# Optimization experiments

Measured on AMD Instinct MI355X. Metric: run time of the kernel, lower is better.

Reference implementation:

```python
import jax, jax.numpy as jnp
import numpy as np

D = 256      # linear_dim
H = 8        # heads
B, S = 4, 2048


def setup_inputs() -> dict:
    key = jax.random.key(0)
    ks = jax.random.split(key, 9)
    scale = 1.0 / np.sqrt(D)
    x = jax.random.normal(ks[0], (B, S, D), dtype=jnp.float32)
    # per-head Linear weights stacked: [H, out, in] (torch Linear layout)
    Wq = jax.random.normal(ks[1], (H, D, D), dtype=jnp.float32) * scale
    bq = jax.random.normal(ks[2], (H, D), dtype=jnp.float32) * scale
    Wk = jax.random.normal(ks[3], (H, D, D), dtype=jnp.float32) * scale
    bk = jax.random.normal(ks[4], (H, D), dtype=jnp.float32) * scale
    Wv = jax.random.normal(ks[5], (H, D, D), dtype=jnp.float32) * scale
    bv = jax.random.normal(ks[6], (H, D), dtype=jnp.float32) * scale
    Wo = jax.random.normal(ks[7], (D, H * D), dtype=jnp.float32) * (1.0 / np.sqrt(H * D))
    bo = jax.random.normal(ks[8], (D,), dtype=jnp.float32) * scale
    return {"x": x, "Wq": Wq, "bq": bq, "Wk": Wk, "bk": bk,
            "Wv": Wv, "bv": bv, "Wo": Wo, "bo": bo}


def reference(x, Wq, bq, Wk, bk, Wv, bv, Wo, bo):
    # Batched per-head projections (torch Linear: y = x @ W.T + b)
    Q = jnp.einsum('bsd,hed->bhse', x, Wq) + bq[None, :, None, :]  # [B,H,S,D]
    K = jnp.einsum('bsd,hed->bhse', x, Wk) + bk[None, :, None, :]
    V = jnp.einsum('bsd,hed->bhse', x, Wv) + bv[None, :, None, :]
    scores = jnp.einsum('bhse,bhte->bhst', Q, K) / jnp.sqrt(jnp.float32(D))  # [B,H,Sq,Sk]
    # FAITHFUL quirk: original softmaxes over dim=1 of [B,S,S] -> the QUERY axis.
    attn = jax.nn.softmax(scores, axis=2)
    Z = jnp.einsum('bhst,bhte->bhse', attn, V)       # [B,H,S,D]
    Z = jnp.transpose(Z, (0, 2, 1, 3)).reshape(B, S, H * D)  # concat heads (head-major order matches torch.cat)
    return jnp.einsum('bsf,of->bso', Z, Wo) + bo
```

## Files before the change

kernel.cpp:

```cpp
#include <hip/hip_runtime.h>
#include <hip/hip_bf16.h>

#define DEV __device__ __forceinline__

typedef __bf16 bf16x8 __attribute__((ext_vector_type(8)));
typedef float f32x4 __attribute__((ext_vector_type(4)));

DEV f32x4 mfma16(bf16x8 a, bf16x8 b, f32x4 c) {
  return __builtin_amdgcn_mfma_f32_16x16x32_bf16(a, b, c, 0, 0, 0);
}

DEV ushort f2bf(float f) {
  union { __hip_bfloat16 h; ushort u; } cv;
  cv.h = __float2bfloat16(f);
  return cv.u;
}
DEV float bf2f(ushort u) {
  union { float f; unsigned v; } cv; cv.v = ((unsigned)u) << 16; return cv.f;
}

DEV float fexp2(float x) { return __builtin_amdgcn_exp2f(x); }

#define GLD16(gp, lp)                                                              \
  __builtin_amdgcn_global_load_lds(                                                \
      (const __attribute__((address_space(1))) unsigned int*)(gp),                 \
      (__attribute__((address_space(3))) unsigned int*)(lp), 16, 0, 0)


__global__ __launch_bounds__(256) void convert_all(
    const float* __restrict__ x, const float* __restrict__ wq,
    const float* __restrict__ wk, const float* __restrict__ wv,
    const float* __restrict__ wo, ushort* __restrict__ dst)
{
  size_t i = ((size_t)blockIdx.x * 256 + threadIdx.x) * 4;
  const float* src; size_t off;
  if (i < (size_t)2097152) { src = x; off = i; }
  else {
    size_t j = i - 2097152;
    unsigned wsel = (unsigned)(j >> 19);
    off = j & 524287;
    src = wsel == 0 ? wq : wsel == 1 ? wk : wsel == 2 ? wv : wo;
  }
  float4 v = *(const float4*)(src + off);
  ushort4 o;
  o.x = f2bf(v.x); o.y = f2bf(v.y); o.z = f2bf(v.z); o.w = f2bf(v.w);
  *(ushort4*)(dst + i) = o;
}

template<int BM, int BN>
__global__ __launch_bounds__(256, 2) void gemm_qkv(
    const ushort* __restrict__ A,
    const ushort* __restrict__ W0, const ushort* __restrict__ W1, const ushort* __restrict__ W2,
    int K,
    const float* __restrict__ b0, const float* __restrict__ b1, const float* __restrict__ b2,
    ushort* __restrict__ Qo, ushort* __restrict__ Ko, ushort* __restrict__ Vo)
{
  constexpr int WM = BM / 2, WN = BN / 2, MF = WM / 16, NF = WN / 16;
  const int n0 = blockIdx.x * BN, m0 = blockIdx.y * BM;
  const int tid = threadIdx.x, lane = tid & 63;
  const int wm = (tid >> 7) & 1, wn = (tid >> 6) & 1;
  const int g = lane >> 4, r15 = lane & 15;

  __shared__ ushort As[BM * 72];
  __shared__ ushort Bs[BN * 72];

  const int p = n0 >> 11;
  const ushort* Bt = (p == 0 ? W0 : p == 1 ? W1 : W2) + (size_t)(n0 & 2047) * K;

  f32x4 acc[MF][NF];
#pragma unroll
  for (int m = 0; m < MF; m++)
#pragma unroll
    for (int n = 0; n < NF; n++) acc[m][n] = (f32x4){0.f, 0.f, 0.f, 0.f};

  for (int k0 = 0; k0 < K; k0 += 64) {
#pragma unroll
    for (int i = 0; i < 4; i++) {
      int ci = tid * 4 + i; int r = ci >> 3, c = ci & 7;
      *(uint4*)&As[r * 72 + c * 8] = *(const uint4*)&A[(size_t)(m0 + r) * K + k0 + c * 8];
      *(uint4*)&Bs[r * 72 + c * 8] = *(const uint4*)&Bt[(size_t)r * K + k0 + c * 8];
    }
    __syncthreads();
    bf16x8 af[MF][2], bfr[NF][2];
#pragma unroll
    for (int m = 0; m < MF; m++)
#pragma unroll
      for (int k2 = 0; k2 < 2; ++k2)
        af[m][k2] = *(const bf16x8*)&As[(wm * WM + m * 16 + r15) * 72 + k2 * 32 + g * 8];
#pragma unroll
    for (int n = 0; n < NF; n++)
#pragma unroll
      for (int k2 = 0; k2 < 2; ++k2)
        bfr[n][k2] = *(const bf16x8*)&Bs[(wn * WN + n * 16 + r15) * 72 + k2 * 32 + g * 8];
#pragma unroll
    for (int k2 = 0; k2 < 2; ++k2)
#pragma unroll
      for (int m = 0; m < MF; m++)
#pragma unroll
        for (int n = 0; n < NF; n++) acc[m][n] = mfma16(af[m][k2], bfr[n][k2], acc[m][n]);
    __syncthreads();
  }

  const float* bias = (p == 0 ? b0 : p == 1 ? b1 : b2);
  const float scl = (p == 0 ? 0.0625f * 1.44269504088896f : 1.0f);
#pragma unroll
  for (int m = 0; m < MF; m++)
#pragma unroll
    for (int n = 0; n < NF; n++)
#pragma unroll
      for (int r = 0; r < 4; r++) {
        int row = m0 + wm * WM + m * 16 + g * 4 + r;
        int col = n0 + wn * WN + n * 16 + r15;
        int ce = col & 2047;
        float v = (acc[m][n][r] + bias[ce]) * scl;
        int b = row >> 11, s = row & 2047, h = ce >> 8, e = ce & 255;
        int bh = b * 8 + h;
        if (p == 0) {
          Qo[((size_t)(bh * 2048 + s) << 8) + e] = f2bf(v);
        } else if (p == 1) {
          int ee = ((((e >> 3) ^ (s & 7)) & 31) << 3) | (e & 7);
          Ko[((size_t)(bh * 2048 + s) << 8) + ee] = f2bf(v);
        } else {
          Vo[(((size_t)bh * 64 + (s >> 5)) << 13) + e * 32 + (s & 31)] = f2bf(v);
        }
      }
}

__global__ __launch_bounds__(256, 2) void gemm_out(
    const ushort* __restrict__ A, const ushort* __restrict__ Bw,
    const float* __restrict__ bias, float* __restrict__ out)
{
  const int n0 = blockIdx.x * 64, m0 = blockIdx.y * 64;
  const int tid = threadIdx.x, lane = tid & 63;
  const int wm = (tid >> 7) & 1, wn = (tid >> 6) & 1;
  const int g = lane >> 4, r15 = lane & 15;

  __shared__ ushort As[64 * 72];
  __shared__ ushort Bs[64 * 72];

  f32x4 acc[2][2];
#pragma unroll
  for (int m = 0; m < 2; m++)
#pragma unroll
    for (int n = 0; n < 2; n++) acc[m][n] = (f32x4){0.f, 0.f, 0.f, 0.f};

  for (int k0 = 0; k0 < 2048; k0 += 64) {
#pragma unroll
    for (int i = 0; i < 2; ++i) {
      int ci = tid * 2 + i, r = ci >> 3, c = ci & 7;
      *(uint4*)&As[r * 72 + c * 8] = *(const uint4*)&A[(size_t)(m0 + r) * 2048 + k0 + c * 8];
      *(uint4*)&Bs[r * 72 + c * 8] = *(const uint4*)&Bw[(size_t)(n0 + r) * 2048 + k0 + c * 8];
    }
    __syncthreads();
    bf16x8 af[2][2], bfr[2][2];
#pragma unroll
    for (int m = 0; m < 2; ++m)
#pragma unroll
      for (int k2 = 0; k2 < 2; ++k2)
        af[m][k2] = *(const bf16x8*)&As[(wm * 32 + m * 16 + r15) * 72 + k2 * 32 + g * 8];
#pragma unroll
    for (int n = 0; n < 2; ++n)
#pragma unroll
      for (int k2 = 0; k2 < 2; ++k2)
        bfr[n][k2] = *(const bf16x8*)&Bs[(wn * 32 + n * 16 + r15) * 72 + k2 * 32 + g * 8];
#pragma unroll
    for (int k2 = 0; k2 < 2; ++k2)
#pragma unroll
      for (int m = 0; m < 2; ++m)
#pragma unroll
        for (int n = 0; n < 2; ++n)
          acc[m][n] = mfma16(af[m][k2], bfr[n][k2], acc[m][n]);
    __syncthreads();
  }

#pragma unroll
  for (int m = 0; m < 2; m++)
#pragma unroll
    for (int n = 0; n < 2; n++)
#pragma unroll
      for (int r = 0; r < 4; r++) {
        int row = m0 + wm * 32 + m * 16 + g * 4 + r;
        int col = n0 + wn * 32 + n * 16 + r15;
        out[(size_t)row * 256 + col] = acc[m][n][r] + bias[col];
      }
}

__global__ __launch_bounds__(256, 2) void attn_p0(
    const ushort* __restrict__ Qb, const ushort* __restrict__ Kb,
    float* __restrict__ lpart)
{
  const int bid = blockIdx.x;
  const int swz = (bid & 7) * 64 + (bid >> 3);
  const int bh = swz >> 4, stile = (swz >> 1) & 7, half = swz & 1;
  const int s0 = stile * 256;
  const int tid = threadIdx.x, lane = tid & 63, w = tid >> 6;
  const int g = lane >> 4, r15 = lane & 15;

  __shared__ __align__(16) ushort Ks[2][8192];

  uint4 qr[4][8];
#pragma unroll
  for (int h = 0; h < 4; ++h) {
    const ushort* qrow = &Qb[((size_t)bh * 2048 + s0 + w * 64 + h * 16 + r15) * 256 + g * 8];
#pragma unroll
    for (int kk = 0; kk < 8; kk++) qr[h][kk] = *(const uint4*)&qrow[kk * 32];
  }
#pragma unroll
  for (int h = 0; h < 4; ++h)
#pragma unroll
    for (int kk = 0; kk < 8; kk++)
      asm volatile("" : "+v"(qr[h][kk].x), "+v"(qr[h][kk].y),
                        "+v"(qr[h][kk].z), "+v"(qr[h][kk].w));

  const ushort* Ktile = Kb + ((size_t)bh << 19);
  const int it0 = half * 32, it1 = it0 + 32;

#pragma unroll
  for (int i = 0; i < 4; ++i)
    GLD16(&Ktile[(size_t)it0 * 8192 + (i * 256 + tid) * 8], &Ks[0][(i * 256 + tid) * 8]);
  asm volatile("s_waitcnt vmcnt(0)" ::: "memory");
  __syncthreads();

  for (int it = it0; it < it1; ++it) {
    const int cur = it & 1;
    if (it < it1 - 1) {
#pragma unroll
      for (int i = 0; i < 4; ++i)
        GLD16(&Ktile[(size_t)(it + 1) * 8192 + (i * 256 + tid) * 8],
              &Ks[cur ^ 1][(i * 256 + tid) * 8]);
    }

#pragma unroll
    for (int n = 0; n < 2; ++n) {
      f32x4 gh[4];
#pragma unroll
      for (int h = 0; h < 4; ++h) gh[h] = (f32x4){0.f, 0.f, 0.f, 0.f};
#pragma unroll
      for (int kk = 0; kk < 8; ++kk) {
        bf16x8 kb = *(const bf16x8*)&Ks[cur][(n * 16 + r15) * 256 + (((kk * 4 + g) ^ (r15 & 7)) << 3)];
        gh[0] = mfma16(*(const bf16x8*)&qr[0][kk], kb, gh[0]);
        gh[1] = mfma16(*(const bf16x8*)&qr[1][kk], kb, gh[1]);
        gh[2] = mfma16(*(const bf16x8*)&qr[2][kk], kb, gh[2]);
        gh[3] = mfma16(*(const bf16x8*)&qr[3][kk], kb, gh[3]);
      }
      float sn = 0.f;
#pragma unroll
      for (int h = 0; h < 4; ++h)
        sn += fexp2(gh[h][0]) + fexp2(gh[h][1]) + fexp2(gh[h][2]) + fexp2(gh[h][3]);
      sn += __shfl_xor(sn, 16);
      sn += __shfl_xor(sn, 32);
      if (g == 0)
        lpart[((size_t)((stile * 4 + w) * 32 + bh) << 11) + it * 32 + n * 16 + r15] = sn;
    }

    asm volatile("s_waitcnt vmcnt(0)" ::: "memory");
    __syncthreads();
  }
}

__global__ __launch_bounds__(256, 2) void attn_p1(
    const ushort* __restrict__ Qb, const ushort* __restrict__ Kb,
    const ushort* __restrict__ Vt, ushort* __restrict__ Zb)
{
  const int bid = blockIdx.x;
  const int swz = (bid & 7) * 64 + (bid >> 3);
  const int bh = swz >> 4, stile = swz & 15;
  const int s0 = stile * 128;
  const int tid = threadIdx.x, lane = tid & 63, w = tid >> 6;
  const int g = lane >> 4, r15 = lane & 15;

  __shared__ __align__(16) ushort Ks[2][8192];
  __shared__ __align__(16) ushort Ps[2][5120];

  bf16x8 q[2][8];
#pragma unroll
  for (int h = 0; h < 2; ++h) {
    const ushort* qrow = &Qb[((size_t)bh * 2048 + s0 + w * 32 + h * 16 + r15) * 256 + g * 8];
#pragma unroll
    for (int kk = 0; kk < 8; kk++) q[h][kk] = *(const bf16x8*)&qrow[kk * 32];
  }

  const ushort* Ktile = Kb + ((size_t)bh << 19);
  const ushort* Vtile = Vt + ((size_t)bh << 19);

  f32x4 acc[8][4];
#pragma unroll
  for (int m = 0; m < 8; m++)
#pragma unroll
    for (int n = 0; n < 4; n++) acc[m][n] = (f32x4){0.f, 0.f, 0.f, 0.f};

#pragma unroll
  for (int i = 0; i < 4; ++i)
    GLD16(&Ktile[(size_t)(i * 256 + tid) * 8], &Ks[0][(i * 256 + tid) * 8]);
  asm volatile("s_waitcnt vmcnt(0)" ::: "memory");
  __syncthreads();

  for (int it = 0; it < 64; ++it) {
    const int cur = it & 1;
    bf16x8 vb[4];
#pragma unroll
    for (int n = 0; n < 4; ++n)
      vb[n] = *(const bf16x8*)&Vtile[(size_t)it * 8192 + (w * 64 + n * 16 + r15) * 32 + g * 8];
    if (it < 63) {
#pragma unroll
      for (int i = 0; i < 4; ++i)
        GLD16(&Ktile[(size_t)(it + 1) * 8192 + (i * 256 + tid) * 8],
              &Ks[cur ^ 1][(i * 256 + tid) * 8]);
    }

#pragma unroll
    for (int h = 0; h < 2; ++h) {
      f32x4 gg[2];
      gg[0] = (f32x4){0.f, 0.f, 0.f, 0.f};
      gg[1] = (f32x4){0.f, 0.f, 0.f, 0.f};
#pragma unroll
      for (int n = 0; n < 2; ++n)
#pragma unroll
        for (int kk = 0; kk < 8; ++kk) {
          bf16x8 kb = *(const bf16x8*)&Ks[cur][(n * 16 + r15) * 256 + (((kk * 4 + g) ^ (r15 & 7)) << 3)];
          gg[n] = mfma16(q[h][kk], kb, gg[n]);
        }
#pragma unroll
      for (int n = 0; n < 2; ++n)
#pragma unroll
        for (int rr = 0; rr < 4; ++rr)
          Ps[cur][(w * 32 + h * 16 + g * 4 + rr) * 40 + n * 16 + r15] = f2bf(fexp2(gg[n][rr]));
    }

    asm volatile("s_waitcnt vmcnt(0)" ::: "memory");
    __syncthreads();

#pragma unroll
    for (int mh = 0; mh < 2; ++mh) {
      bf16x8 pa[4];
#pragma unroll
      for (int m = 0; m < 4; ++m)
        pa[m] = *(const bf16x8*)&Ps[cur][((mh * 4 + m) * 16 + r15) * 40 + g * 8];
#pragma unroll
      for (int n = 0; n < 4; ++n)
#pragma unroll
        for (int m = 0; m < 4; ++m)
          acc[mh * 4 + m][n] = mfma16(pa[m], vb[n], acc[mh * 4 + m][n]);
    }
  }

  const int b = bh >> 3, h = bh & 7;
#pragma unroll
  for (int m = 0; m < 8; m++)
#pragma unroll
    for (int n = 0; n < 4; n++)
#pragma unroll
      for (int rr = 0; rr < 4; rr++) {
        int sl = m * 16 + g * 4 + rr;
        int el = w * 64 + n * 16 + r15;
        Zb[((size_t)(b * 2048 + s0 + sl)) * 2048 + h * 256 + el] = f2bf(acc[m][n][rr]);
      }
}

__global__ __launch_bounds__(256) void vscale(
    ushort* __restrict__ Vt, const float* __restrict__ lp)
{
  const int tt = blockIdx.x, bh = blockIdx.y, tid = threadIdx.x;
  const int t = tid & 31, pg = tid >> 5;
  __shared__ float red[256];
  __shared__ float cinv[32];
  float s = 0.f;
  for (int p = pg * 4; p < pg * 4 + 4; ++p)
    s += lp[(((size_t)p * 32 + bh) << 11) + tt * 32 + t];
  red[tid] = s;
  __syncthreads();
  if (tid < 32) {
    float tot = 0.f;
#pragma unroll
    for (int i = 0; i < 8; ++i) tot += red[tid + i * 32];
    cinv[tid] = 1.0f / tot;
  }
  __syncthreads();
  size_t base = (((size_t)bh * 64 + tt) << 13) + (size_t)tid * 32;
  ushort buf[32];
#pragma unroll
  for (int i = 0; i < 4; ++i) *(uint4*)&buf[i * 8] = *(const uint4*)&Vt[base + i * 8];
#pragma unroll
  for (int j = 0; j < 32; ++j) buf[j] = f2bf(bf2f(buf[j]) * cinv[j]);
#pragma unroll
  for (int i = 0; i < 4; ++i) *(uint4*)&Vt[base + i * 8] = *(const uint4*)&buf[i * 8];
}

extern "C" void kernel_launch(void* const* d_in, const int* in_sizes, int n_in,
                              void* d_out, int out_size, void* d_ws, size_t ws_size,
                              hipStream_t stream) {
  const float* x  = (const float*)d_in[0];
  const float* Wq = (const float*)d_in[1];
  const float* bq = (const float*)d_in[2];
  const float* Wk = (const float*)d_in[3];
  const float* bk = (const float*)d_in[4];
  const float* Wv = (const float*)d_in[5];
  const float* bv = (const float*)d_in[6];
  const float* Wo = (const float*)d_in[7];
  const float* bo = (const float*)d_in[8];

  if (ws_size < (size_t)176160768) return;

  char* ws = (char*)d_ws;
  ushort* bfb = (ushort*)ws;
  ushort* xb  = bfb;
  ushort* wqb = bfb + 2097152;
  ushort* wkb = bfb + 2621440;
  ushort* wvb = bfb + 3145728;
  ushort* wob = bfb + 3670016;
  ushort* Qb = (ushort*)(ws + 8388608);
  ushort* Kb = (ushort*)(ws + 41943040);
  ushort* Vt = (ushort*)(ws + 75497472);
  ushort* Zb = (ushort*)(ws + 109051904);
  float*  lp = (float*)(ws + 142606336);
  float* out = (float*)d_out;

  convert_all<<<4096, 256, 0, stream>>>(x, Wq, Wk, Wv, Wo, bfb);
  gemm_qkv<128, 128><<<dim3(48, 64), 256, 0, stream>>>(
      xb, wqb, wkb, wvb, 256, bq, bk, bv, Qb, Kb, Vt);
  attn_p0<<<512, 256, 0, stream>>>(Qb, Kb, lp);
  vscale<<<dim3(64, 32), 256, 0, stream>>>(Vt, lp);
  attn_p1<<<512, 256, 0, stream>>>(Qb, Kb, Vt, Zb);
  gemm_out<<<dim3(4, 128), 256, 0, stream>>>(Zb, wob, bo, out);
}
```

Before: 319.7 us.

## Triple-buffer K tiles in attention and widen QKV GEMM k-step to 128

The attention kernel's K staging moves from double to triple buffering, prefetching two tiles ahead. The full vmcnt(0) wait plus __syncthreads is replaced by a partial vmcnt wait and a raw s_barrier, so global loads stay in flight across iterations. Separately, the QKV projection GEMM now stages 128-wide k slices in shared memory instead of 64, halving the number of barriers. The trade-off is more LDS per block, which could reduce occupancy, and the vmcnt counts must exactly match the number of loads issued per iteration.

```diff
diff --git a/kernel.cpp b/kernel.cpp
--- a/kernel.cpp
+++ b/kernel.cpp
@@ -61,8 +61,8 @@
   const int wm = (tid >> 7) & 1, wn = (tid >> 6) & 1;
   const int g = lane >> 4, r15 = lane & 15;
 
-  __shared__ ushort As[BM * 72];
-  __shared__ ushort Bs[BN * 72];
+  __shared__ ushort As[BM * 136];
+  __shared__ ushort Bs[BN * 136];
 
   const int p = n0 >> 11;
   const ushort* Bt = (p == 0 ? W0 : p == 1 ? W1 : W2) + (size_t)(n0 & 2047) * K;
@@ -73,31 +73,28 @@
 #pragma unroll
     for (int n = 0; n < NF; n++) acc[m][n] = (f32x4){0.f, 0.f, 0.f, 0.f};
 
-  for (int k0 = 0; k0 < K; k0 += 64) {
-#pragma unroll
-    for (int i = 0; i < 4; i++) {
-      int ci = tid * 4 + i; int r = ci >> 3, c = ci & 7;
-      *(uint4*)&As[r * 72 + c * 8] = *(const uint4*)&A[(size_t)(m0 + r) * K + k0 + c * 8];
-      *(uint4*)&Bs[r * 72 + c * 8] = *(const uint4*)&Bt[(size_t)r * K + k0 + c * 8];
+  for (int k0 = 0; k0 < K; k0 += 128) {
+#pragma unroll
+    for (int i = 0; i < 8; i++) {
+      int ci = tid * 8 + i; int r = ci >> 4, c = ci & 15;
+      *(uint4*)&As[r * 136 + c * 8] = *(const uint4*)&A[(size_t)(m0 + r) * K + k0 + c * 8];
+      *(uint4*)&Bs[r * 136 + c * 8] = *(const uint4*)&Bt[(size_t)r * K + k0 + c * 8];
     }
     __syncthreads();
-    bf16x8 af[MF][2], bfr[NF][2];
-#pragma unroll
-    for (int m = 0; m < MF; m++)
-#pragma unroll
-      for (int k2 = 0; k2 < 2; ++k2)
-        af[m][k2] = *(const bf16x8*)&As[(wm * WM + m * 16 + r15) * 72 + k2 * 32 + g * 8];
-#pragma unroll
-    for (int n = 0; n < NF; n++)
-#pragma unroll
-      for (int k2 = 0; k2 < 2; ++k2)
-        bfr[n][k2] = *(const bf16x8*)&Bs[(wn * WN + n * 16 + r15) * 72 + k2 * 32 + g * 8];
-#pragma unroll
-    for (int k2 = 0; k2 < 2; ++k2)
+#pragma unroll
+    for (int k2 = 0; k2 < 4; ++k2) {
+      bf16x8 af[MF], bfr[NF];
 #pragma unroll
       for (int m = 0; m < MF; m++)
-#pragma unroll
-        for (int n = 0; n < NF; n++) acc[m][n] = mfma16(af[m][k2], bfr[n][k2], acc[m][n]);
+        af[m] = *(const bf16x8*)&As[(wm * WM + m * 16 + r15) * 136 + k2 * 32 + g * 8];
+#pragma unroll
+      for (int n = 0; n < NF; n++)
+        bfr[n] = *(const bf16x8*)&Bs[(wn * WN + n * 16 + r15) * 136 + k2 * 32 + g * 8];
+#pragma unroll
+      for (int m = 0; m < MF; m++)
+#pragma unroll
+        for (int n = 0; n < NF; n++) acc[m][n] = mfma16(af[m], bfr[n], acc[m][n]);
+    }
     __syncthreads();
   }
 
@@ -269,7 +266,7 @@
   const int tid = threadIdx.x, lane = tid & 63, w = tid >> 6;
   const int g = lane >> 4, r15 = lane & 15;
 
-  __shared__ __align__(16) ushort Ks[2][8192];
+  __shared__ __align__(16) ushort Ks[3][8192];
   __shared__ __align__(16) ushort Ps[2][5120];
 
   bf16x8 q[2][8];
@@ -292,20 +289,27 @@
 #pragma unroll
   for (int i = 0; i < 4; ++i)
     GLD16(&Ktile[(size_t)(i * 256 + tid) * 8], &Ks[0][(i * 256 + tid) * 8]);
-  asm volatile("s_waitcnt vmcnt(0)" ::: "memory");
-  __syncthreads();
+#pragma unroll
+  for (int i = 0; i < 4; ++i)
+    GLD16(&Ktile[(size_t)8192 + (i * 256 + tid) * 8], &Ks[1][(i * 256 + tid) * 8]);
+  asm volatile("s_waitcnt vmcnt(4)" ::: "memory");
+  __builtin_amdgcn_s_barrier();
+  __builtin_amdgcn_sched_barrier(0);
 
   for (int it = 0; it < 64; ++it) {
-    const int cur = it & 1;
+    const int kcur = it % 3;
+    const int pcur = it & 1;
     bf16x8 vb[4];
 #pragma unroll
     for (int n = 0; n < 4; ++n)
       vb[n] = *(const bf16x8*)&Vtile[(size_t)it * 8192 + (w * 64 + n * 16 + r15) * 32 + g * 8];
-    if (it < 63) {
+    {
+      const int nx = it < 62 ? it + 2 : 63;
+      const int knxt = (it + 2) % 3;
 #pragma unroll
       for (int i = 0; i < 4; ++i)
-        GLD16(&Ktile[(size_t)(it + 1) * 8192 + (i * 256 + tid) * 8],
-              &Ks[cur ^ 1][(i * 256 + tid) * 8]);
+        GLD16(&Ktile[(size_t)nx * 8192 + (i * 256 + tid) * 8],
+              &Ks[knxt][(i * 256 + tid) * 8]);
     }
 
 #pragma unroll
@@ -317,25 +321,27 @@
       for (int n = 0; n < 2; ++n)
 #pragma unroll
         for (int kk = 0; kk < 8; ++kk) {
-          bf16x8 kb = *(const bf16x8*)&Ks[cur][(n * 16 + r15) * 256 + (((kk * 4 + g) ^ (r15 & 7)) << 3)];
+          bf16x8 kb = *(const bf16x8*)&Ks[kcur][(n * 16 + r15) * 256 + (((kk * 4 + g) ^ (r15 & 7)) << 3)];
           gg[n] = mfma16(q[h][kk], kb, gg[n]);
         }
 #pragma unroll
       for (int n = 0; n < 2; ++n)
 #pragma unroll
         for (int rr = 0; rr < 4; ++rr)
-          Ps[cur][(w * 32 + h * 16 + g * 4 + rr) * 40 + n * 16 + r15] = f2bf(fexp2(gg[n][rr]));
-    }
-
-    asm volatile("s_waitcnt vmcnt(0)" ::: "memory");
-    __syncthreads();
+          Ps[pcur][(w * 32 + h * 16 + g * 4 + rr) * 40 + n * 16 + r15] = f2bf(fexp2(gg[n][rr]));
+    }
+
+    asm volatile("s_waitcnt lgkmcnt(0)" ::: "memory");
+    asm volatile("s_waitcnt vmcnt(8)" ::: "memory");
+    __builtin_amdgcn_s_barrier();
+    __builtin_amdgcn_sched_barrier(0);
 
 #pragma unroll
     for (int mh = 0; mh < 2; ++mh) {
       bf16x8 pa[4];
 #pragma unroll
       for (int m = 0; m < 4; ++m)
-        pa[m] = *(const bf16x8*)&Ps[cur][((mh * 4 + m) * 16 + r15) * 40 + g * 8];
+        pa[m] = *(const bf16x8*)&Ps[pcur][((mh * 4 + m) * 16 + r15) * 40 + g * 8];
 #pragma unroll
       for (int n = 0; n < 4; ++n)
 #pragma unroll
```

Measured after the change: 523.5 us. +63.7%, slower.
